# Optimization experiments

Hardware: AMD Instinct MI355X
Metric: run time of the kernel (lower is better)

Reference implementation:

```python
import jax, jax.numpy as jnp
import numpy as np
import math

DIM = 2048
NUM_HEADS = 32
HEAD_DIM = DIM // NUM_HEADS  # 64; HEAD_DIM//2 == NUM_HEADS (required by original rope broadcasting)
SEQ_LEN = 2048
BATCH = 2
ROPE_BASE = 10000.0


def apply_rope(inputs, positions):
    # Faithful to original: positions is [L]; sinusoid broadcasts to [1, L, H/2, 1]
    # and then multiplies [B, L, N, H/2] -- the original code relies on N == H/2.
    head_dim = inputs.shape[-1]
    fraction = 2.0 * jnp.arange(head_dim // 2, dtype=inputs.dtype) / head_dim
    timescale = ROPE_BASE ** fraction                      # [H/2]
    sinusoid = positions[:, None] / timescale[None, None, :]  # [1, L, H/2]
    sinusoid = sinusoid[..., None]                         # [1, L, H/2, 1]
    sin = jnp.sin(sinusoid)
    cos = jnp.cos(sinusoid)
    first, second = jnp.split(inputs, 2, axis=-1)          # each [B, L, N, H/2]
    return jnp.concatenate([first * cos - second * sin,
                            second * cos + first * sin], axis=-1)


def setup_inputs() -> dict:
    key = jax.random.key(0)
    ks = jax.random.split(key, 9)
    s = 0.02
    inp = {
        'x': jax.random.normal(ks[0], (BATCH, SEQ_LEN, DIM), dtype=jnp.float32),
        'wq_w': jax.random.normal(ks[1], (DIM, DIM), dtype=jnp.float32) * s,
        'wq_b': jnp.zeros((DIM,), dtype=jnp.float32),
        'wk_w': jax.random.normal(ks[2], (DIM, DIM), dtype=jnp.float32) * s,
        'wk_b': jnp.zeros((DIM,), dtype=jnp.float32),
        'wv_w': jax.random.normal(ks[3], (DIM, DIM), dtype=jnp.float32) * s,
        'wv_b': jnp.zeros((DIM,), dtype=jnp.float32),
        'wo_w': jax.random.normal(ks[4], (DIM, DIM), dtype=jnp.float32) * s,
        'wo_b': jnp.zeros((DIM,), dtype=jnp.float32),
    }
    return inp


def reference(x, wq_w, wq_b, wk_w, wk_b, wv_w, wv_b, wo_w, wo_b):
    B, L, _ = x.shape
    N, H = NUM_HEADS, HEAD_DIM
    q = (x @ wq_w.T + wq_b).reshape(B, L, N, H)
    k = (x @ wk_w.T + wk_b).reshape(B, L, N, H)
    v = (x @ wv_w.T + wv_b).reshape(B, L, N, H)
    positions = jnp.arange(L, dtype=x.dtype)
    q = apply_rope(q, positions)
    k = apply_rope(k, positions)
    # [B, N, L, H]
    q = q.transpose(0, 2, 1, 3)
    k = k.transpose(0, 2, 1, 3)
    v = v.transpose(0, 2, 1, 3)
    scale = math.sqrt(H)
    scores = jnp.einsum('bnqh,bnkh->bnqk', q, k) / scale   # [B, N, L, L]
    causal = jnp.tril(jnp.ones((L, L), dtype=bool))
    scores = jnp.where(causal[None, None], scores, -jnp.inf)
    attn = jax.nn.softmax(scores, axis=-1)
    context = jnp.einsum('bnqk,bnkh->bnqh', attn, v)        # [B, N, L, H]
    context = context.transpose(0, 2, 1, 3).reshape(B, L, DIM)
    return context @ wo_w.T + wo_b
```

## Files before the change

### kernel.cpp

```cpp
#include <hip/hip_runtime.h>
#include <stdint.h>

#define D_MODEL 2048
#define SEQLEN  2048

typedef float f32x4  __attribute__((ext_vector_type(4)));
typedef float f32x16 __attribute__((ext_vector_type(16)));
typedef int   i32x4  __attribute__((ext_vector_type(4)));
typedef short s16x4  __attribute__((ext_vector_type(4)));
typedef __bf16 bf16x8 __attribute__((ext_vector_type(8)));

__device__ __forceinline__ unsigned short f2bf(float f) {
  union { float f; uint32_t u; } x; x.f = f;
  uint32_t r = (x.u + 0x7FFFu + ((x.u >> 16) & 1u)) >> 16;
  return (unsigned short)r;
}

__device__ __forceinline__ bf16x8 as_bf16x8(i32x4 v) {
  union { i32x4 i; bf16x8 b; } u; u.i = v; return u.b;
}

#define MFMA16(acc, a, b) \
  acc = __builtin_amdgcn_mfma_f32_16x16x32_bf16(as_bf16x8(a), as_bf16x8(b), acc, 0, 0, 0)
#define MFMA32(acc, a, b) \
  acc = __builtin_amdgcn_mfma_f32_32x32x16_bf16(as_bf16x8(a), as_bf16x8(b), acc, 0, 0, 0)

__device__ __forceinline__ void gload16(const void* g, void* lds) {
  __builtin_amdgcn_global_load_lds(
      (const __attribute__((address_space(1))) unsigned int*)(uintptr_t)g,
      (__attribute__((address_space(3))) unsigned int*)(uint32_t)(uintptr_t)lds,
      16, 0, 0);
}

__global__ void cvt_bf16_k(const float* __restrict__ in,
                           unsigned short* __restrict__ out, int n4) {
  int i = blockIdx.x * 256 + threadIdx.x;
  if (i < n4) {
    f32x4 v = *(const f32x4*)&in[(size_t)i * 4];
    s16x4 o;
#pragma unroll
    for (int j = 0; j < 4; ++j) o[j] = (short)f2bf(v[j]);
    *(s16x4*)&out[(size_t)i * 4] = o;
  }
}

template <int BM, int BN, int NW, int G, int MODE>
__global__ __launch_bounds__(NW * 64) void gemm2p(
    const unsigned short* __restrict__ A,
    const unsigned short* __restrict__ W0,
    const unsigned short* __restrict__ W1,
    const unsigned short* __restrict__ W2,
    const float* __restrict__ bias0,
    const float* __restrict__ bias1,
    const float* __restrict__ bias2,
    unsigned short* __restrict__ O0,
    unsigned short* __restrict__ O1,
    unsigned short* __restrict__ O2,
    float* __restrict__ Of) {
  constexpr int PLANE_E = (BM + BN) * 32;
  __shared__ alignas(16) unsigned short L[4 * PLANE_E];

  const int t = threadIdx.x;
  const int w = t >> 6, l = t & 63;
  const int wm = w >> 1, wn = w & 1;
  const int band = l >> 4, ln = l & 15;

  const int bx = blockIdx.x;
  const int m0 = blockIdx.y * BM;

  const unsigned short* Wm;
  const float* bias;
  int nloc, mat;
  if constexpr (MODE == 0) {
    mat = bx >> 4;
    nloc = (bx & 15) * BN;
    Wm = mat == 0 ? W0 : (mat == 1 ? W1 : W2);
    bias = mat == 0 ? bias0 : (mat == 1 ? bias1 : bias2);
  } else {
    mat = 0;
    nloc = bx * BN;
    Wm = W0;
    bias = bias0;
  }

  auto stage = [&](int p, int ktile, int b) {
    unsigned short* dst = L + (b * 2 + p) * PLANE_E;
    const int kcol = ktile * 64 + p * 32;
#pragma unroll
    for (int i = 0; i < G; ++i) {
      const int idx = w * G + i;
      const int row = idx * 16 + (l >> 2);
      const int gblk = (l & 3) ^ ((row >> 1) & 3);
      const unsigned short* src =
          (idx * 16 < BM) ? &A[(size_t)(m0 + row) * D_MODEL + kcol + gblk * 8]
                          : &Wm[(size_t)(nloc + row - BM) * D_MODEL + kcol + gblk * 8];
      gload16(src, dst + idx * 512);
    }
  };

  f32x4 acc[4][4] = {};

  stage(0, 0, 0);
  stage(1, 0, 0);
  if constexpr (G == 3) asm volatile("s_waitcnt vmcnt(3)" ::: "memory");
  else                  asm volatile("s_waitcnt vmcnt(4)" ::: "memory");
  __builtin_amdgcn_s_barrier();

  for (int kt = 0; kt < 32; ++kt) {
    const int rb = kt & 1;
    const int ktn = (kt + 1) & 31;
#pragma unroll
    for (int p = 0; p < 2; ++p) {
      const unsigned short* Apl = L + (rb * 2 + p) * PLANE_E;
      const unsigned short* Bpl = Apl + BM * 32;
      i32x4 av[4], bv[4];
#pragma unroll
      for (int mf = 0; mf < 4; ++mf) {
        const int row = wm * 64 + mf * 16 + ln;
        av[mf] = *(const i32x4*)&Apl[row * 32 + (((band ^ (row >> 1)) & 3) << 3)];
      }
#pragma unroll
      for (int nf = 0; nf < 4; ++nf) {
        const int row = wn * 64 + nf * 16 + ln;
        bv[nf] = *(const i32x4*)&Bpl[row * 32 + (((band ^ (row >> 1)) & 3) << 3)];
      }
      stage(p, ktn, rb ^ 1);
      __builtin_amdgcn_s_barrier();
      asm volatile("s_waitcnt lgkmcnt(0)" ::: "memory");
      __builtin_amdgcn_sched_barrier(0);
      __builtin_amdgcn_s_setprio(1);
#pragma unroll
      for (int mf = 0; mf < 4; ++mf)
#pragma unroll
        for (int nf = 0; nf < 4; ++nf)
          MFMA16(acc[mf][nf], av[mf], bv[nf]);
      __builtin_amdgcn_s_setprio(0);
      if constexpr (G == 3) asm volatile("s_waitcnt vmcnt(3)" ::: "memory");
      else                  asm volatile("s_waitcnt vmcnt(4)" ::: "memory");
      __builtin_amdgcn_s_barrier();
    }
  }
  asm volatile("s_waitcnt vmcnt(0)" ::: "memory");

  float bb[4];
#pragma unroll
  for (int nf = 0; nf < 4; ++nf) bb[nf] = bias[nloc + wn * 64 + nf * 16 + ln];

  if constexpr (MODE == 0) {
    unsigned short* Out = mat == 0 ? O0 : (mat == 1 ? O1 : O2);
    const bool rope = (mat < 2);
    const int head = (nloc + wn * 64) >> 6;
    const float ts = powf(10000.0f, (float)head * (1.0f / 32.0f));
#pragma unroll
    for (int mf = 0; mf < 4; ++mf) {
#pragma unroll
      for (int r = 0; r < 4; ++r) {
        const int row = m0 + wm * 64 + mf * 16 + band * 4 + r;
        float vals[4];
#pragma unroll
        for (int nf = 0; nf < 4; ++nf) vals[nf] = acc[mf][nf][r] + bb[nf];
        if (rope) {
          const float pos = (float)(row & (SEQLEN - 1));
          float sv, cv;
          sincosf(pos / ts, &sv, &cv);
#pragma unroll
          for (int pp = 0; pp < 2; ++pp) {
            const float f0 = vals[pp], s0 = vals[pp + 2];
            vals[pp]     = f0 * cv - s0 * sv;
            vals[pp + 2] = s0 * cv + f0 * sv;
          }
        }
#pragma unroll
        for (int nf = 0; nf < 4; ++nf)
          Out[(size_t)row * D_MODEL + nloc + wn * 64 + nf * 16 + ln] = f2bf(vals[nf]);
      }
    }
  } else {
#pragma unroll
    for (int mf = 0; mf < 4; ++mf)
#pragma unroll
      for (int r = 0; r < 4; ++r) {
        const int row = m0 + wm * 64 + mf * 16 + band * 4 + r;
#pragma unroll
        for (int nf = 0; nf < 4; ++nf)
          Of[(size_t)row * D_MODEL + nloc + wn * 64 + nf * 16 + ln] =
              acc[mf][nf][r] + bb[nf];
      }
  }
}

__global__ __launch_bounds__(256) void attn_fwd(
    const unsigned short* __restrict__ Q, const unsigned short* __restrict__ K,
    const unsigned short* __restrict__ V, unsigned short* __restrict__ O) {
  __shared__ alignas(16) unsigned short Ks[2][64 * 64];
  __shared__ alignas(16) unsigned short Vt[2][64 * 80];

  const int t = threadIdx.x;
  const int w = t >> 6, l = t & 63;
  const int l31 = l & 31, t5 = l >> 5;
  const int bx = blockIdx.x, head = blockIdx.y, b = blockIdx.z;
  const int h0 = head * 64;
  const size_t rb = (size_t)b * SEQLEN;

  const int vg = t & 7, vrow = t >> 3;
  const int kdr = l >> 3, kdb = l & 7;

  for (int pi = 0; pi < 2; ++pi) {
    const int qt = pi ? (15 - bx) : bx;
    const int q0 = qt * 128;
    const int qg = q0 + w * 32 + l31;

    i32x4 qf[4];
#pragma unroll
    for (int hk = 0; hk < 4; ++hk)
      qf[hk] = *(const i32x4*)&Q[(rb + qg) * D_MODEL + h0 + hk * 16 + t5 * 8];

    f32x16 oacc[2] = {};
    float lsum = 0.f;
    const int nkt = qt * 2 + 2;

    {
#pragma unroll
      for (int i = 0; i < 2; ++i) {
        const int drow = (i * 4 + w) * 8 + kdr;
        const int sblk = kdb ^ (drow & 7);
        gload16(&K[(rb + drow) * D_MODEL + h0 + sblk * 8], &Ks[0][(i * 4 + w) * 512]);
      }
      i32x4 vv[2];
#pragma unroll
      for (int i = 0; i < 2; ++i)
        vv[i] = *(const i32x4*)&V[(rb + i * 32 + vrow) * D_MODEL + h0 + vg * 8];
      asm volatile("s_waitcnt vmcnt(0)" ::: "memory");
#pragma unroll
      for (int i = 0; i < 2; ++i) {
        const int r = i * 32 + vrow, c8 = vg * 8;
        union { i32x4 v; unsigned short s[8]; } u; u.v = vv[i];
#pragma unroll
        for (int j = 0; j < 8; ++j) Vt[0][(c8 + j) * 80 + (r ^ c8)] = u.s[j];
      }
    }
    __syncthreads();

    for (int kt = 0; kt < nkt; ++kt) {
      const int cur = kt & 1, nxt = cur ^ 1;
      const int k0 = kt * 64;
      const bool more = (kt + 1 < nkt);

      i32x4 vv[2];
      if (more) {
        const int k1 = k0 + 64;
#pragma unroll
        for (int i = 0; i < 2; ++i) {
          const int drow = (i * 4 + w) * 8 + kdr;
          const int sblk = kdb ^ (drow & 7);
          gload16(&K[(rb + k1 + drow) * D_MODEL + h0 + sblk * 8],
                  &Ks[nxt][(i * 4 + w) * 512]);
        }
#pragma unroll
        for (int i = 0; i < 2; ++i)
          vv[i] = *(const i32x4*)&V[(rb + k1 + i * 32 + vrow) * D_MODEL + h0 + vg * 8];
      }

      f32x16 sacc[2] = {};
#pragma unroll
      for (int kvf = 0; kvf < 2; ++kvf) {
        const int krow = kvf * 32 + l31;
#pragma unroll
        for (int hk = 0; hk < 4; ++hk) {
          i32x4 a = *(const i32x4*)&Ks[cur][krow * 64 + ((2 * hk + t5) ^ (krow & 7)) * 8];
          MFMA32(sacc[kvf], a, qf[hk]);
        }
      }

      const bool needmask = (k0 + 64 > q0 + w * 32);
      uint32_t W[2][4][2];
#pragma unroll
      for (int kvf = 0; kvf < 2; ++kvf)
#pragma unroll
        for (int g = 0; g < 4; ++g)
#pragma unroll
          for (int p = 0; p < 2; ++p) {
            uint32_t wd = 0;
#pragma unroll
            for (int e = 0; e < 2; ++e) {
              const int reg = 4 * g + 2 * p + e;
              const int kvl = kvf * 32 + 8 * g + 4 * t5 + 2 * p + e;
              float pv = __expf(sacc[kvf][reg] * 0.125f);
              if (needmask && (k0 + kvl > qg)) pv = 0.f;
              lsum += pv;
              wd |= (uint32_t)f2bf(pv) << (16 * e);
            }
            W[kvf][g][p] = wd;
          }

#pragma unroll
      for (int ks = 0; ks < 4; ++ks) {
        const int kvf = ks >> 1;
        const int gA = 2 * (ks & 1), gB = gA + 1;
        const uint32_t O0 = t5 ? W[kvf][gB][0] : W[kvf][gA][0];
        const uint32_t O1 = t5 ? W[kvf][gB][1] : W[kvf][gA][1];
        const uint32_t E0 = t5 ? W[kvf][gA][0] : W[kvf][gB][0];
        const uint32_t E1 = t5 ? W[kvf][gA][1] : W[kvf][gB][1];
        const uint32_t X0 = (uint32_t)__shfl_xor((int)E0, 32);
        const uint32_t X1 = (uint32_t)__shfl_xor((int)E1, 32);
        i32x4 pf;
        pf[0] = (int)(t5 ? X0 : O0);
        pf[1] = (int)(t5 ? X1 : O1);
        pf[2] = (int)(t5 ? O0 : X0);
        pf[3] = (int)(t5 ? O1 : X1);
#pragma unroll
        for (int hf = 0; hf < 2; ++hf) {
          const int h = hf * 32 + l31;
          i32x4 vb = *(const i32x4*)&Vt[cur][h * 80 + ((ks * 16 + t5 * 8) ^ ((h >> 3) * 8))];
          MFMA32(oacc[hf], pf, vb);
        }
      }

      if (more) {
        asm volatile("s_waitcnt vmcnt(0)" ::: "memory");
#pragma unroll
        for (int i = 0; i < 2; ++i) {
          const int r = i * 32 + vrow, c8 = vg * 8;
          union { i32x4 v; unsigned short s[8]; } u; u.v = vv[i];
#pragma unroll
          for (int j = 0; j < 8; ++j) Vt[nxt][(c8 + j) * 80 + (r ^ c8)] = u.s[j];
        }
      }
      __syncthreads();
    }

    lsum += __shfl_xor(lsum, 32);
    const float inv = 1.0f / lsum;

#pragma unroll
    for (int g2 = 0; g2 < 4; ++g2)
#pragma unroll
      for (int rr = 0; rr < 4; ++rr) {
        const int rowl = rr + 8 * g2 + 4 * t5;
        const float invr = __shfl(inv, (l & 32) + rowl);
        const size_t gr = rb + q0 + w * 32 + rowl;
#pragma unroll
        for (int hf = 0; hf < 2; ++hf)
          O[gr * D_MODEL + h0 + hf * 32 + l31] = f2bf(oacc[hf][4 * g2 + rr] * invr);
      }
  }
}

extern "C" void kernel_launch(void* const* d_in, const int* in_sizes, int n_in,
                              void* d_out, int out_size, void* d_ws, size_t ws_size,
                              hipStream_t stream) {
  const float* x    = (const float*)d_in[0];
  const float* wq_w = (const float*)d_in[1];
  const float* wq_b = (const float*)d_in[2];
  const float* wk_w = (const float*)d_in[3];
  const float* wk_b = (const float*)d_in[4];
  const float* wv_w = (const float*)d_in[5];
  const float* wv_b = (const float*)d_in[6];
  const float* wo_w = (const float*)d_in[7];
  const float* wo_b = (const float*)d_in[8];
  float* out = (float*)d_out;

  unsigned short* ws  = (unsigned short*)d_ws;
  unsigned short* xb  = ws;
  unsigned short* wqb = xb  + 8388608;
  unsigned short* wkb = wqb + 4194304;
  unsigned short* wvb = wkb + 4194304;
  unsigned short* wob = wvb + 4194304;
  unsigned short* qb  = wob + 4194304;
  unsigned short* kb  = qb  + 8388608;
  unsigned short* vb  = kb  + 8388608;
  unsigned short* cb  = xb;

  cvt_bf16_k<<<8192, 256, 0, stream>>>(x, xb, 2097152);
  cvt_bf16_k<<<4096, 256, 0, stream>>>(wq_w, wqb, 1048576);
  cvt_bf16_k<<<4096, 256, 0, stream>>>(wk_w, wkb, 1048576);
  cvt_bf16_k<<<4096, 256, 0, stream>>>(wv_w, wvb, 1048576);
  cvt_bf16_k<<<4096, 256, 0, stream>>>(wo_w, wob, 1048576);

  gemm2p<128, 128, 4, 4, 0><<<dim3(48, 32), 256, 0, stream>>>(
      xb, wqb, wkb, wvb, wq_b, wk_b, wv_b, qb, kb, vb, nullptr);

  attn_fwd<<<dim3(8, 32, 2), 256, 0, stream>>>(qb, kb, vb, cb);

  gemm2p<128, 128, 4, 4, 1><<<dim3(16, 32), 256, 0, stream>>>(
      cb, wob, nullptr, nullptr, wo_b, nullptr, nullptr,
      nullptr, nullptr, nullptr, out);
}
```

Before: 284.2 us.

## Enlarge GEMM tiles to 256x128 with 8 waves and use packed bf16/permlane swaps in attention

The projection GEMMs move from 128x128 tiles with 4 waves to 256x128 tiles with 8 waves. Each k-step is split into two MFMA phases, so the B fragments are reused across twice as many A rows, which cuts global and LDS traffic per flop. In attention, the manual bf16 rounding and packing is replaced by v_cvt_pk_bf16_f32. The shuffle-plus-select exchange between half-waves is replaced by v_permlane32_swap. The cost is more barriers per k-step, more LDS per block and fewer blocks in the grid (768 and 256).

```diff
diff --git a/kernel.cpp b/kernel.cpp
--- a/kernel.cpp
+++ b/kernel.cpp
@@ -14,6 +14,12 @@
   union { float f; uint32_t u; } x; x.f = f;
   uint32_t r = (x.u + 0x7FFFu + ((x.u >> 16) & 1u)) >> 16;
   return (unsigned short)r;
+}
+
+__device__ __forceinline__ uint32_t cvtpk(float lo, float hi) {
+  uint32_t r;
+  asm("v_cvt_pk_bf16_f32 %0, %1, %2" : "=v"(r) : "v"(lo), "v"(hi));
+  return r;
 }
 
 __device__ __forceinline__ bf16x8 as_bf16x8(i32x4 v) {
@@ -44,8 +50,8 @@
   }
 }
 
-template <int BM, int BN, int NW, int G, int MODE>
-__global__ __launch_bounds__(NW * 64) void gemm2p(
+template <int MODE>
+__global__ __launch_bounds__(512) void gemm4p(
     const unsigned short* __restrict__ A,
     const unsigned short* __restrict__ W0,
     const unsigned short* __restrict__ W1,
@@ -57,7 +63,7 @@
     unsigned short* __restrict__ O1,
     unsigned short* __restrict__ O2,
     float* __restrict__ Of) {
-  constexpr int PLANE_E = (BM + BN) * 32;
+  constexpr int PLANE_E = 384 * 32;
   __shared__ alignas(16) unsigned short L[4 * PLANE_E];
 
   const int t = threadIdx.x;
@@ -66,77 +72,85 @@
   const int band = l >> 4, ln = l & 15;
 
   const int bx = blockIdx.x;
-  const int m0 = blockIdx.y * BM;
+  const int m0 = blockIdx.y * 256;
 
   const unsigned short* Wm;
   const float* bias;
   int nloc, mat;
   if constexpr (MODE == 0) {
     mat = bx >> 4;
-    nloc = (bx & 15) * BN;
+    nloc = (bx & 15) * 128;
     Wm = mat == 0 ? W0 : (mat == 1 ? W1 : W2);
     bias = mat == 0 ? bias0 : (mat == 1 ? bias1 : bias2);
   } else {
     mat = 0;
-    nloc = bx * BN;
+    nloc = bx * 128;
     Wm = W0;
     bias = bias0;
   }
 
-  auto stage = [&](int p, int ktile, int b) {
+  auto stage1 = [&](int p, int ktile, int b, int i) {
     unsigned short* dst = L + (b * 2 + p) * PLANE_E;
+    const int idx = w * 3 + i;
+    const int row = idx * 16 + (l >> 2);
+    const int gblk = (l & 3) ^ ((row >> 1) & 3);
     const int kcol = ktile * 64 + p * 32;
-#pragma unroll
-    for (int i = 0; i < G; ++i) {
-      const int idx = w * G + i;
-      const int row = idx * 16 + (l >> 2);
-      const int gblk = (l & 3) ^ ((row >> 1) & 3);
-      const unsigned short* src =
-          (idx * 16 < BM) ? &A[(size_t)(m0 + row) * D_MODEL + kcol + gblk * 8]
-                          : &Wm[(size_t)(nloc + row - BM) * D_MODEL + kcol + gblk * 8];
-      gload16(src, dst + idx * 512);
-    }
+    const unsigned short* src =
+        (idx < 16) ? &A[(size_t)(m0 + row) * D_MODEL + kcol + gblk * 8]
+                   : &Wm[(size_t)(nloc + row - 256) * D_MODEL + kcol + gblk * 8];
+    gload16(src, dst + idx * 512);
   };
+  auto ld = [&](const unsigned short* pl, int r) {
+    return *(const i32x4*)&pl[r * 32 + (((band ^ (r >> 1)) & 3) << 3)];
+  };
 
   f32x4 acc[4][4] = {};
 
-  stage(0, 0, 0);
-  stage(1, 0, 0);
-  if constexpr (G == 3) asm volatile("s_waitcnt vmcnt(3)" ::: "memory");
-  else                  asm volatile("s_waitcnt vmcnt(4)" ::: "memory");
+#pragma unroll
+  for (int i = 0; i < 3; ++i) stage1(0, 0, 0, i);
+#pragma unroll
+  for (int i = 0; i < 3; ++i) stage1(1, 0, 0, i);
+  asm volatile("s_waitcnt vmcnt(3)" ::: "memory");
   __builtin_amdgcn_s_barrier();
 
   for (int kt = 0; kt < 32; ++kt) {
     const int rb = kt & 1;
     const int ktn = (kt + 1) & 31;
 #pragma unroll
-    for (int p = 0; p < 2; ++p) {
-      const unsigned short* Apl = L + (rb * 2 + p) * PLANE_E;
-      const unsigned short* Bpl = Apl + BM * 32;
-      i32x4 av[4], bv[4];
-#pragma unroll
-      for (int mf = 0; mf < 4; ++mf) {
-        const int row = wm * 64 + mf * 16 + ln;
-        av[mf] = *(const i32x4*)&Apl[row * 32 + (((band ^ (row >> 1)) & 3) << 3)];
-      }
-#pragma unroll
-      for (int nf = 0; nf < 4; ++nf) {
-        const int row = wn * 64 + nf * 16 + ln;
-        bv[nf] = *(const i32x4*)&Bpl[row * 32 + (((band ^ (row >> 1)) & 3) << 3)];
-      }
-      stage(p, ktn, rb ^ 1);
+    for (int kh = 0; kh < 2; ++kh) {
+      const unsigned short* pl = L + (rb * 2 + kh) * PLANE_E;
+      i32x4 bv[4], av[2];
+#pragma unroll
+      for (int nf = 0; nf < 4; ++nf) bv[nf] = ld(pl, 256 + wn * 64 + nf * 16 + ln);
+#pragma unroll
+      for (int mf = 0; mf < 2; ++mf) av[mf] = ld(pl, wm * 64 + mf * 16 + ln);
+      stage1(kh, ktn, rb ^ 1, 0);
+      stage1(kh, ktn, rb ^ 1, 1);
       __builtin_amdgcn_s_barrier();
       asm volatile("s_waitcnt lgkmcnt(0)" ::: "memory");
       __builtin_amdgcn_sched_barrier(0);
       __builtin_amdgcn_s_setprio(1);
 #pragma unroll
-      for (int mf = 0; mf < 4; ++mf)
+      for (int mf = 0; mf < 2; ++mf)
 #pragma unroll
         for (int nf = 0; nf < 4; ++nf)
           MFMA16(acc[mf][nf], av[mf], bv[nf]);
       __builtin_amdgcn_s_setprio(0);
-      if constexpr (G == 3) asm volatile("s_waitcnt vmcnt(3)" ::: "memory");
-      else                  asm volatile("s_waitcnt vmcnt(4)" ::: "memory");
+      __builtin_amdgcn_s_barrier();
+#pragma unroll
+      for (int mf = 0; mf < 2; ++mf) av[mf] = ld(pl, wm * 64 + (2 + mf) * 16 + ln);
+      stage1(kh, ktn, rb ^ 1, 2);
+      __builtin_amdgcn_s_barrier();
+      asm volatile("s_waitcnt lgkmcnt(0)" ::: "memory");
+      __builtin_amdgcn_sched_barrier(0);
+      __builtin_amdgcn_s_setprio(1);
+#pragma unroll
+      for (int mf = 0; mf < 2; ++mf)
+#pragma unroll
+        for (int nf = 0; nf < 4; ++nf)
+          MFMA16(acc[2 + mf][nf], av[mf], bv[nf]);
+      __builtin_amdgcn_s_setprio(0);
+      asm volatile("s_waitcnt vmcnt(3)" ::: "memory");
       __builtin_amdgcn_s_barrier();
     }
   }
@@ -152,13 +166,13 @@
     const int head = (nloc + wn * 64) >> 6;
     const float ts = powf(10000.0f, (float)head * (1.0f / 32.0f));
 #pragma unroll
-    for (int mf = 0; mf < 4; ++mf) {
+    for (int am = 0; am < 4; ++am) {
 #pragma unroll
       for (int r = 0; r < 4; ++r) {
-        const int row = m0 + wm * 64 + mf * 16 + band * 4 + r;
+        const int row = m0 + wm * 64 + am * 16 + band * 4 + r;
         float vals[4];
 #pragma unroll
-        for (int nf = 0; nf < 4; ++nf) vals[nf] = acc[mf][nf][r] + bb[nf];
+        for (int nf = 0; nf < 4; ++nf) vals[nf] = acc[am][nf][r] + bb[nf];
         if (rope) {
           const float pos = (float)(row & (SEQLEN - 1));
           float sv, cv;
@@ -177,14 +191,14 @@
     }
   } else {
 #pragma unroll
-    for (int mf = 0; mf < 4; ++mf)
+    for (int am = 0; am < 4; ++am)
 #pragma unroll
       for (int r = 0; r < 4; ++r) {
-        const int row = m0 + wm * 64 + mf * 16 + band * 4 + r;
+        const int row = m0 + wm * 64 + am * 16 + band * 4 + r;
 #pragma unroll
         for (int nf = 0; nf < 4; ++nf)
           Of[(size_t)row * D_MODEL + nloc + wn * 64 + nf * 16 + ln] =
-              acc[mf][nf][r] + bb[nf];
+              acc[am][nf][r] + bb[nf];
       }
   }
 }
@@ -280,34 +294,28 @@
         for (int g = 0; g < 4; ++g)
 #pragma unroll
           for (int p = 0; p < 2; ++p) {
-            uint32_t wd = 0;
+            float pv[2];
 #pragma unroll
             for (int e = 0; e < 2; ++e) {
               const int reg = 4 * g + 2 * p + e;
               const int kvl = kvf * 32 + 8 * g + 4 * t5 + 2 * p + e;
-              float pv = __expf(sacc[kvf][reg] * 0.125f);
-              if (needmask && (k0 + kvl > qg)) pv = 0.f;
-              lsum += pv;
-              wd |= (uint32_t)f2bf(pv) << (16 * e);
+              pv[e] = __expf(sacc[kvf][reg] * 0.125f);
+              if (needmask && (k0 + kvl > qg)) pv[e] = 0.f;
+              lsum += pv[e];
             }
-            W[kvf][g][p] = wd;
+            W[kvf][g][p] = cvtpk(pv[0], pv[1]);
           }
 
 #pragma unroll
       for (int ks = 0; ks < 4; ++ks) {
         const int kvf = ks >> 1;
         const int gA = 2 * (ks & 1), gB = gA + 1;
-        const uint32_t O0 = t5 ? W[kvf][gB][0] : W[kvf][gA][0];
-        const uint32_t O1 = t5 ? W[kvf][gB][1] : W[kvf][gA][1];
-        const uint32_t E0 = t5 ? W[kvf][gA][0] : W[kvf][gB][0];
-        const uint32_t E1 = t5 ? W[kvf][gA][1] : W[kvf][gB][1];
-        const uint32_t X0 = (uint32_t)__shfl_xor((int)E0, 32);
-        const uint32_t X1 = (uint32_t)__shfl_xor((int)E1, 32);
+        uint32_t a0 = W[kvf][gA][0], b0 = W[kvf][gB][0];
+        uint32_t a1 = W[kvf][gA][1], b1 = W[kvf][gB][1];
+        asm("v_permlane32_swap_b32 %0, %1" : "+v"(a0), "+v"(b0));
+        asm("v_permlane32_swap_b32 %0, %1" : "+v"(a1), "+v"(b1));
         i32x4 pf;
-        pf[0] = (int)(t5 ? X0 : O0);
-        pf[1] = (int)(t5 ? X1 : O1);
-        pf[2] = (int)(t5 ? O0 : X0);
-        pf[3] = (int)(t5 ? O1 : X1);
+        pf[0] = (int)a0; pf[1] = (int)a1; pf[2] = (int)b0; pf[3] = (int)b1;
 #pragma unroll
         for (int hf = 0; hf < 2; ++hf) {
           const int h = hf * 32 + l31;
@@ -377,12 +385,12 @@
   cvt_bf16_k<<<4096, 256, 0, stream>>>(wv_w, wvb, 1048576);
   cvt_bf16_k<<<4096, 256, 0, stream>>>(wo_w, wob, 1048576);
 
-  gemm2p<128, 128, 4, 4, 0><<<dim3(48, 32), 256, 0, stream>>>(
+  gemm4p<0><<<dim3(48, 16), 512, 0, stream>>>(
       xb, wqb, wkb, wvb, wq_b, wk_b, wv_b, qb, kb, vb, nullptr);
 
   attn_fwd<<<dim3(8, 32, 2), 256, 0, stream>>>(qb, kb, vb, cb);
 
-  gemm2p<128, 128, 4, 4, 1><<<dim3(16, 32), 256, 0, stream>>>(
+  gemm4p<1><<<dim3(16, 16), 512, 0, stream>>>(
       cb, wob, nullptr, nullptr, wo_b, nullptr, nullptr,
       nullptr, nullptr, nullptr, out);
 }
```

Result: faster. 268.0 us (-5.7%).
